# Optimization experiments

Measured on AMD Instinct MI355X. Metric: run time of the kernel, lower is better.

The kernel has to match this reference:

```python
import jax, jax.numpy as jnp
import numpy as np

DIM = 512
HIDDEN = 2048
BATCH = 16384
NUM_VECTORS = 3


def _mlp(z, W1, b1, W2, b2, W3, b3):
    # 3-layer tanh MLP: dim -> hidden -> hidden -> dim
    h = jnp.tanh(z @ W1.T + b1)
    h = jnp.tanh(h @ W2.T + b2)
    return h @ W3.T + b3


def setup_inputs() -> dict:
    key = jax.random.key(0)
    ks = jax.random.split(key, 10)
    t = jnp.zeros((1,), dtype=jnp.float32)
    augmented_state = jax.random.normal(ks[0], (BATCH, DIM + 1), dtype=jnp.float32)
    epsilons = jax.random.normal(ks[1], (NUM_VECTORS, BATCH, DIM), dtype=jnp.float32)
    # Xavier-normal-ish init with gain 0.1 (final layer randomized instead of the
    # original zero-init so outputs/grads are non-trivial for kernel testing).
    def xavier(k, fan_out, fan_in, gain=0.1):
        std = gain * np.sqrt(2.0 / (fan_in + fan_out))
        return (jax.random.normal(k, (fan_out, fan_in), dtype=jnp.float32) * std)
    W1 = xavier(ks[2], HIDDEN, DIM)
    b1 = jnp.zeros((HIDDEN,), dtype=jnp.float32)
    W2 = xavier(ks[3], HIDDEN, HIDDEN)
    b2 = jnp.zeros((HIDDEN,), dtype=jnp.float32)
    W3 = xavier(ks[4], DIM, HIDDEN)
    b3 = jnp.zeros((DIM,), dtype=jnp.float32)
    return {"t": t, "augmented_state": augmented_state, "epsilons": epsilons,
            "W1": W1, "b1": b1, "W2": W2, "b2": b2, "W3": W3, "b3": b3}


def reference(t, augmented_state, epsilons, W1, b1, W2, b2, W3, b3):
    dim = W1.shape[1]
    z = augmented_state[:, :dim]                      # [B, dim]
    dz_dt = _mlp(z, W1, b1, W2, b2, W3, b3)           # [B, dim]
    # torch code computes g = d(sum f(z))/dz = J^T @ 1 (same for every loop
    # iteration since only epsilon is resampled), then averages (g * eps).sum(1).
    g = jax.grad(lambda zz: _mlp(zz, W1, b1, W2, b2, W3, b3).sum())(z)  # [B, dim]
    num_vectors = epsilons.shape[0]
    trace = jnp.einsum('kbd,bd->b', epsilons, g)[:, None] / num_vectors  # [B, 1]
    return jnp.concatenate([dz_dt, trace], axis=1)    # [B, dim+1]
```

## Files before the change

kernel.cpp:

```cpp
#include <hip/hip_runtime.h>
#include <hip/hip_bf16.h>
#include <stdint.h>

#define DIM 512
#define HIDDEN 2048
#define BATCH 16384

using bf16 = __hip_bfloat16;
typedef float f32x4 __attribute__((ext_vector_type(4)));
typedef short bf16x8 __attribute__((ext_vector_type(8)));

__device__ __forceinline__ float bf2f(bf16 x) { return __bfloat162float(x); }
__device__ __forceinline__ bf16 f2bf(float x) { return __float2bfloat16(x); }

__device__ __forceinline__ float fast_tanh(float x) {
    float e = __expf(2.0f * x);
    return 1.0f - 2.0f * __builtin_amdgcn_rcpf(e + 1.0f);
}

__device__ __forceinline__ f32x4 mfma16(bf16x8 a, bf16x8 b, f32x4 c) {
    return __builtin_amdgcn_mfma_f32_16x16x32_bf16(a, b, c, 0, 0, 0);
}

__device__ __forceinline__ void BARP() {
    __builtin_amdgcn_sched_barrier(0);
    __builtin_amdgcn_s_barrier();
    __builtin_amdgcn_sched_barrier(0);
}
__device__ __forceinline__ void LGK0_SB() {
    asm volatile("s_waitcnt lgkmcnt(0)" ::: "memory");
    __builtin_amdgcn_sched_barrier(0);
}
__device__ __forceinline__ void VMC4() {
    asm volatile("s_waitcnt vmcnt(4)" ::: "memory");
}

__device__ __forceinline__ void stage_half(const bf16* __restrict__ G, int grow0,
                                           int Kdim, int kbase, bf16* lds,
                                           int elem_base, int wave, int srow4, int gs8)
{
#pragma unroll
    for (int i = 0; i < 2; ++i) {
        const int q = wave * 2 + i;
        const bf16* ga = G + (size_t)(grow0 + q * 16 + srow4) * Kdim + kbase + gs8;
        __builtin_amdgcn_global_load_lds(
            (const __attribute__((address_space(1))) void*)ga,
            (__attribute__((address_space(3))) void*)(lds + elem_base + q * 512), 16, 0, 0);
    }
}

template <int MODE>
__global__ __launch_bounds__(512, 2)
void gemm8(const bf16* __restrict__ A, const bf16* __restrict__ Bt,
           int M, int N, int K,
           const float* __restrict__ bias,
           bf16* __restrict__ out1, bf16* __restrict__ out2,
           const float* __restrict__ u3, const bf16* __restrict__ h1s)
{
    __shared__ bf16 lds[65536];
    const int tid  = threadIdx.x;
    const int lane = tid & 63;
    const int wave = tid >> 6;

    const int nwg = gridDim.x * gridDim.y;
    const int bid = blockIdx.y * gridDim.x + blockIdx.x;
    const int cpx = nwg >> 3;
    const int sw  = (bid & 7) * cpx + (bid >> 3);
    const int nbn = N >> 8;
    const int bm  = sw / nbn;
    const int bn  = sw % nbn;
    const int row0 = bm << 8;
    const int col0 = bn << 8;

    const int wr = wave >> 2;
    const int wc = wave & 3;
    const int l15 = lane & 15;

    const int slotl    = (((lane >> 4) ^ ((l15 >> 1) & 3)) << 4);
    const int laneoffA = (wr * 128 + l15) * 64 + slotl;
    const int laneoffB = (wc * 64  + l15) * 64 + slotl;
    const int srow4 = lane >> 2;
    const int gs8   = (((lane & 3) ^ ((lane >> 3) & 3)) << 3);

    const char* ldsc = (const char*)lds;
    f32x4 acc[8][4] = {};
    bf16x8 af[4], bfv[4];

    stage_half(A,  row0, K, 0,  lds, 0,     wave, srow4, gs8);
    stage_half(Bt, col0, K, 0,  lds, 16384, wave, srow4, gs8);
    stage_half(A,  row0, K, 32, lds, 8192,  wave, srow4, gs8);
    stage_half(Bt, col0, K, 32, lds, 24576, wave, srow4, gs8);
    VMC4(); BARP();

    const int KT = K >> 6;
    for (int t = 0; t < KT; ++t) {
        const int cur = t & 1;
        const int cb  = cur << 16;
        const int ce  = (cur ^ 1) << 15;
        const int knt = ((t + 1 < KT) ? t + 1 : 0) << 6;

#pragma unroll
        for (int j = 0; j < 4; ++j)
            af[j] = *(const bf16x8*)(ldsc + cb + j * 1024 + laneoffA);
#pragma unroll
        for (int j = 0; j < 4; ++j)
            bfv[j] = *(const bf16x8*)(ldsc + cb + 32768 + j * 1024 + laneoffB);
        stage_half(A, row0, K, knt, lds, ce, wave, srow4, gs8);
        BARP(); LGK0_SB();
        __builtin_amdgcn_s_setprio(1);
#pragma unroll
        for (int m = 0; m < 4; ++m)
#pragma unroll
            for (int n = 0; n < 4; ++n)
                acc[m][n] = mfma16(af[m], bfv[n], acc[m][n]);
        __builtin_amdgcn_s_setprio(0);
        BARP();

#pragma unroll
        for (int j = 0; j < 4; ++j)
            af[j] = *(const bf16x8*)(ldsc + cb + (4 + j) * 1024 + laneoffA);
        stage_half(Bt, col0, K, knt, lds, ce + 16384, wave, srow4, gs8);
        BARP(); LGK0_SB();
        __builtin_amdgcn_s_setprio(1);
#pragma unroll
        for (int m = 0; m < 4; ++m)
#pragma unroll
            for (int n = 0; n < 4; ++n)
                acc[4 + m][n] = mfma16(af[m], bfv[n], acc[4 + m][n]);
        __builtin_amdgcn_s_setprio(0);
        VMC4();
        BARP();

#pragma unroll
        for (int j = 0; j < 4; ++j)
            af[j] = *(const bf16x8*)(ldsc + cb + 16384 + j * 1024 + laneoffA);
#pragma unroll
        for (int j = 0; j < 4; ++j)
            bfv[j] = *(const bf16x8*)(ldsc + cb + 49152 + j * 1024 + laneoffB);
        stage_half(A, row0, K, knt + 32, lds, ce + 8192, wave, srow4, gs8);
        BARP(); LGK0_SB();
        __builtin_amdgcn_s_setprio(1);
#pragma unroll
        for (int m = 0; m < 4; ++m)
#pragma unroll
            for (int n = 0; n < 4; ++n)
                acc[m][n] = mfma16(af[m], bfv[n], acc[m][n]);
        __builtin_amdgcn_s_setprio(0);
        BARP();

#pragma unroll
        for (int j = 0; j < 4; ++j)
            af[j] = *(const bf16x8*)(ldsc + cb + 16384 + (4 + j) * 1024 + laneoffA);
        stage_half(Bt, col0, K, knt + 32, lds, ce + 24576, wave, srow4, gs8);
        BARP(); LGK0_SB();
        __builtin_amdgcn_s_setprio(1);
#pragma unroll
        for (int m = 0; m < 4; ++m)
#pragma unroll
            for (int n = 0; n < 4; ++n)
                acc[4 + m][n] = mfma16(af[m], bfv[n], acc[4 + m][n]);
        __builtin_amdgcn_s_setprio(0);
        VMC4();
        BARP();
    }

    const int c4 = (lane >> 4) << 2;
#pragma unroll
    for (int m = 0; m < 8; ++m) {
        const int growb = row0 + wr * 128 + m * 16 + c4;
#pragma unroll
        for (int n = 0; n < 4; ++n) {
            const int gcol = col0 + wc * 64 + n * 16 + l15;
            const float bz = (MODE == 3) ? 0.0f : bias[gcol];
            const float uu = (MODE == 1) ? u3[gcol] : 0.0f;
#pragma unroll
            for (int r = 0; r < 4; ++r) {
                const size_t idx = (size_t)(growb + r) * N + gcol;
                const float cv = acc[m][n][r];
                if (MODE == 0) {
                    out1[idx] = f2bf(fast_tanh(cv + bz));
                } else if (MODE == 1) {
                    float v = fast_tanh(cv + bz);
                    out1[idx] = f2bf(v);
                    out2[idx] = f2bf(uu * (1.0f - v * v));
                } else {
                    float h = bf2f(h1s[idx]);
                    out1[idx] = f2bf(cv * (1.0f - h * h));
                }
            }
        }
    }
}

template <int MODE>
__global__ __launch_bounds__(256)
void gemm_bt(const bf16* __restrict__ A, const bf16* __restrict__ Bt,
             int M, int N, int K,
             const float* __restrict__ bias,
             float* __restrict__ outF,
             const float* __restrict__ esum)
{
    __shared__ __align__(128) bf16 As[128 * 64];
    __shared__ __align__(128) bf16 Bs[128 * 64];

    const int tid  = threadIdx.x;
    const int lane = tid & 63;
    const int wave = tid >> 6;

    const int nwg = gridDim.x * gridDim.y;
    const int bid = blockIdx.y * gridDim.x + blockIdx.x;
    const int cpx = nwg >> 3;
    const int sw  = (bid & 7) * cpx + (bid >> 3);
    const int nbn = N >> 7;
    const int bm  = sw / nbn;
    const int bn  = sw % nbn;
    const int row0 = bm << 7;
    const int col0 = bn << 7;

    const int wr = wave >> 1;
    const int wc = wave & 1;

    f32x4 acc[4][4] = {};

    const int srow  = lane >> 3;
    const int sslot = lane & 7;

    const int KT = K >> 6;
    for (int kt = 0; kt < KT; ++kt) {
        const int k0 = kt << 6;
        __syncthreads();
#pragma unroll
        for (int i = 0; i < 4; ++i) {
            const int q   = wave * 4 + i;
            const int row = q * 8 + srow;
            const int gs  = sslot ^ (row & 7);
            const bf16* ga = A  + (size_t)(row0 + row) * K + (k0 + gs * 8);
            const bf16* gb = Bt + (size_t)(col0 + row) * K + (k0 + gs * 8);
            __builtin_amdgcn_global_load_lds(
                (const __attribute__((address_space(1))) void*)ga,
                (__attribute__((address_space(3))) void*)(As + q * 512), 16, 0, 0);
            __builtin_amdgcn_global_load_lds(
                (const __attribute__((address_space(1))) void*)gb,
                (__attribute__((address_space(3))) void*)(Bs + q * 512), 16, 0, 0);
        }
        __syncthreads();

#pragma unroll
        for (int half = 0; half < 2; ++half) {
            const int kb = half * 4 + (lane >> 4);
            bf16x8 af[4], bfr[4];
#pragma unroll
            for (int m = 0; m < 4; ++m) {
                const int ar = wr * 64 + m * 16 + (lane & 15);
                af[m] = *(const bf16x8*)((const char*)As + ar * 128 + ((kb ^ (ar & 7)) << 4));
            }
#pragma unroll
            for (int n = 0; n < 4; ++n) {
                const int br = wc * 64 + n * 16 + (lane & 15);
                bfr[n] = *(const bf16x8*)((const char*)Bs + br * 128 + ((kb ^ (br & 7)) << 4));
            }
#pragma unroll
            for (int m = 0; m < 4; ++m)
#pragma unroll
                for (int n = 0; n < 4; ++n)
                    acc[m][n] = mfma16(af[m], bfr[n], acc[m][n]);
        }
    }

    const int c_lo = lane & 15;
    const int c_hi = lane >> 4;
    if (MODE == 2) {
#pragma unroll
        for (int m = 0; m < 4; ++m)
#pragma unroll
            for (int n = 0; n < 4; ++n)
#pragma unroll
                for (int r = 0; r < 4; ++r) {
                    const int grow = row0 + wr * 64 + m * 16 + c_hi * 4 + r;
                    const int gcol = col0 + wc * 64 + n * 16 + c_lo;
                    outF[(size_t)grow * 513 + gcol] = acc[m][n][r] + bias[gcol];
                }
    } else {
#pragma unroll
        for (int m = 0; m < 4; ++m) {
#pragma unroll
            for (int r = 0; r < 4; ++r) {
                const int grow = row0 + wr * 64 + m * 16 + c_hi * 4 + r;
                float s = 0.f;
#pragma unroll
                for (int n = 0; n < 4; ++n) {
                    const int gcol = col0 + wc * 64 + n * 16 + c_lo;
                    s += acc[m][n][r] * esum[(size_t)grow * 512 + gcol];
                }
                s += __shfl_xor(s, 1);
                s += __shfl_xor(s, 2);
                s += __shfl_xor(s, 4);
                s += __shfl_xor(s, 8);
                if (c_lo == 0)
                    atomicAdd(outF + (size_t)grow * 513 + 512, s * (1.0f / 3.0f));
            }
        }
    }
}


__global__ void eps_reduce(const float* __restrict__ eps, float* __restrict__ esum, int n)
{
    const float4* e0 = (const float4*)eps;
    const float4* e1 = (const float4*)(eps + (size_t)n);
    const float4* e2 = (const float4*)(eps + 2 * (size_t)n);
    float4* o = (float4*)esum;
    const int n4 = n >> 2;
    const int stride = gridDim.x * blockDim.x;
    for (int i = blockIdx.x * blockDim.x + threadIdx.x; i < n4; i += stride) {
        float4 a = e0[i], b = e1[i], c = e2[i];
        o[i] = make_float4(a.x + b.x + c.x, a.y + b.y + c.y,
                           a.z + b.z + c.z, a.w + b.w + c.w);
    }
}

__global__ void z_convert(const float* __restrict__ aug, bf16* __restrict__ zb,
                          float* __restrict__ out)
{
    const int stride = gridDim.x * blockDim.x;
    for (int i = blockIdx.x * blockDim.x + threadIdx.x; i < BATCH * DIM; i += stride) {
        const int b = i >> 9, d = i & 511;
        zb[i] = f2bf(aug[(size_t)b * 513 + d]);
        if (d == 0) out[(size_t)b * 513 + 512] = 0.f;
    }
}

__global__ void conv_bf16(const float* __restrict__ src, bf16* __restrict__ dst, int n)
{
    const int stride = gridDim.x * blockDim.x;
    for (int i = blockIdx.x * blockDim.x + threadIdx.x; i < n; i += stride)
        dst[i] = f2bf(src[i]);
}

__global__ void transpose_bf16(const float* __restrict__ src, bf16* __restrict__ dst,
                               int R, int C)
{
    __shared__ float t[32][33];
    const int bx = blockIdx.x * 32;
    const int by = blockIdx.y * 32;
    const int tx = threadIdx.x & 31;
    const int ty = threadIdx.x >> 5;
#pragma unroll
    for (int j = 0; j < 32; j += 8)
        t[ty + j][tx] = src[(size_t)(by + ty + j) * C + (bx + tx)];
    __syncthreads();
#pragma unroll
    for (int j = 0; j < 32; j += 8)
        dst[(size_t)(bx + ty + j) * R + (by + tx)] = f2bf(t[tx][ty + j]);
}

__global__ void colsum(const float* __restrict__ W3, float* __restrict__ u3)
{
    const int j = blockIdx.x * blockDim.x + threadIdx.x;
    if (j >= HIDDEN) return;
    float s = 0.f;
    for (int i = 0; i < DIM; ++i) s += W3[(size_t)i * HIDDEN + j];
    u3[j] = s;
}

extern "C" void kernel_launch(void* const* d_in, const int* in_sizes, int n_in,
                              void* d_out, int out_size, void* d_ws, size_t ws_size,
                              hipStream_t stream)
{
    const float* aug = (const float*)d_in[1];
    const float* eps = (const float*)d_in[2];
    const float* W1  = (const float*)d_in[3];
    const float* b1  = (const float*)d_in[4];
    const float* W2  = (const float*)d_in[5];
    const float* b2  = (const float*)d_in[6];
    const float* W3  = (const float*)d_in[7];
    const float* b3  = (const float*)d_in[8];
    float* out = (float*)d_out;

    char* ws = (char*)d_ws;
    size_t off = 0;
    auto alloc = [&](size_t bytes) {
        char* p = ws + off;
        off += (bytes + 255) & ~(size_t)255;
        return p;
    };
    bf16*  zb   = (bf16*)alloc((size_t)BATCH * DIM * 2);
    bf16*  h1   = (bf16*)alloc((size_t)BATCH * HIDDEN * 2);
    bf16*  h2   = (bf16*)alloc((size_t)BATCH * HIDDEN * 2);
    bf16*  d2   = (bf16*)alloc((size_t)BATCH * HIDDEN * 2);
    float* esum = (float*)alloc((size_t)BATCH * DIM * 4);
    bf16*  W1b  = (bf16*)alloc((size_t)HIDDEN * DIM * 2);
    bf16*  W2b  = (bf16*)alloc((size_t)HIDDEN * HIDDEN * 2);
    bf16*  W3b  = (bf16*)alloc((size_t)DIM * HIDDEN * 2);
    bf16*  W2t  = (bf16*)alloc((size_t)HIDDEN * HIDDEN * 2);
    bf16*  W1t  = (bf16*)alloc((size_t)DIM * HIDDEN * 2);
    float* u3   = (float*)alloc((size_t)HIDDEN * 4);
    bf16*  d1   = h2;

    eps_reduce<<<2048, 256, 0, stream>>>(eps, esum, BATCH * DIM);
    z_convert<<<2048, 256, 0, stream>>>(aug, zb, out);
    conv_bf16<<<1024, 256, 0, stream>>>(W1, W1b, HIDDEN * DIM);
    conv_bf16<<<2048, 256, 0, stream>>>(W2, W2b, HIDDEN * HIDDEN);
    conv_bf16<<<1024, 256, 0, stream>>>(W3, W3b, DIM * HIDDEN);
    transpose_bf16<<<dim3(HIDDEN / 32, HIDDEN / 32), 256, 0, stream>>>(W2, W2t, HIDDEN, HIDDEN);
    transpose_bf16<<<dim3(DIM / 32, HIDDEN / 32), 256, 0, stream>>>(W1, W1t, HIDDEN, DIM);
    colsum<<<HIDDEN / 256, 256, 0, stream>>>(W3, u3);

    dim3 g8(BATCH / 256, HIDDEN / 256);
    dim3 gSml(BATCH / 128, DIM / 128);
    gemm8<0><<<g8, 512, 0, stream>>>(zb, W1b, BATCH, HIDDEN, DIM, b1,
                                     h1, nullptr, nullptr, nullptr);
    gemm8<1><<<g8, 512, 0, stream>>>(h1, W2b, BATCH, HIDDEN, HIDDEN, b2,
                                     h2, d2, u3, nullptr);
    gemm_bt<2><<<gSml, 256, 0, stream>>>(h2, W3b, BATCH, DIM, HIDDEN, b3, out, nullptr);
    gemm8<3><<<g8, 512, 0, stream>>>(d2, W2t, BATCH, HIDDEN, HIDDEN, nullptr,
                                     d1, nullptr, nullptr, h1);
    gemm_bt<4><<<gSml, 256, 0, stream>>>(d1, W1t, BATCH, DIM, HIDDEN, nullptr, out, esum);
}
```

Measured before the change: 666.2 us.

## Restructure GEMM main loop into register-prefetched pipeline with one barrier per k-tile

Replaces the four-phase loop, which had a barrier before each MFMA group, with a pipeline that prefetches the next LDS fragments into a second set of registers while the current MFMAs run. Partial lgkmcnt waits replace full drains, and all global-to-LDS staging for tile t+2 is issued after a single barrier per k-tile. The aim is to cut barrier stalls and hide LDS read latency behind MFMA work. The cost is more live registers (four fragment arrays), which may pressure occupancy, and a full vmcnt(0) drain each iteration.

After: 667.5 us. No clear change (+0.2%).

```diff
diff --git a/kernel.cpp b/kernel.cpp
--- a/kernel.cpp
+++ b/kernel.cpp
@@ -27,13 +27,9 @@
     __builtin_amdgcn_s_barrier();
     __builtin_amdgcn_sched_barrier(0);
 }
-__device__ __forceinline__ void LGK0_SB() {
-    asm volatile("s_waitcnt lgkmcnt(0)" ::: "memory");
-    __builtin_amdgcn_sched_barrier(0);
-}
-__device__ __forceinline__ void VMC4() {
-    asm volatile("s_waitcnt vmcnt(4)" ::: "memory");
-}
+#define LGKM(N) do { asm volatile("s_waitcnt lgkmcnt(" #N ")" ::: "memory"); \
+                     __builtin_amdgcn_sched_barrier(0); } while (0)
+#define VMCNT(N) asm volatile("s_waitcnt vmcnt(" #N ")" ::: "memory")
 
 __device__ __forceinline__ void stage_half(const bf16* __restrict__ G, int grow0,
                                            int Kdim, int kbase, bf16* lds,
@@ -84,84 +80,95 @@
 
     const char* ldsc = (const char*)lds;
     f32x4 acc[8][4] = {};
-    bf16x8 af[4], bfv[4];
+    bf16x8 A03[4], A47[4], B0[4], B1[4];
+
+    const int KT = K >> 6;
 
     stage_half(A,  row0, K, 0,  lds, 0,     wave, srow4, gs8);
     stage_half(Bt, col0, K, 0,  lds, 16384, wave, srow4, gs8);
     stage_half(A,  row0, K, 32, lds, 8192,  wave, srow4, gs8);
     stage_half(Bt, col0, K, 32, lds, 24576, wave, srow4, gs8);
-    VMC4(); BARP();
-
-    const int KT = K >> 6;
+    stage_half(A,  row0, K, 64, lds, 32768 + 0,     wave, srow4, gs8);
+    stage_half(Bt, col0, K, 64, lds, 32768 + 16384, wave, srow4, gs8);
+    stage_half(A,  row0, K, 96, lds, 32768 + 8192,  wave, srow4, gs8);
+    stage_half(Bt, col0, K, 96, lds, 32768 + 24576, wave, srow4, gs8);
+    VMCNT(8);
+    BARP();
+#pragma unroll
+    for (int j = 0; j < 4; ++j)
+        A03[j] = *(const bf16x8*)(ldsc + j * 1024 + laneoffA);
+#pragma unroll
+    for (int j = 0; j < 4; ++j)
+        B0[j]  = *(const bf16x8*)(ldsc + 32768 + j * 1024 + laneoffB);
+
     for (int t = 0; t < KT; ++t) {
-        const int cur = t & 1;
-        const int cb  = cur << 16;
-        const int ce  = (cur ^ 1) << 15;
-        const int knt = ((t + 1 < KT) ? t + 1 : 0) << 6;
-
-#pragma unroll
-        for (int j = 0; j < 4; ++j)
-            af[j] = *(const bf16x8*)(ldsc + cb + j * 1024 + laneoffA);
-#pragma unroll
-        for (int j = 0; j < 4; ++j)
-            bfv[j] = *(const bf16x8*)(ldsc + cb + 32768 + j * 1024 + laneoffB);
-        stage_half(A, row0, K, knt, lds, ce, wave, srow4, gs8);
-        BARP(); LGK0_SB();
+        const int cb = (t & 1) << 16;
+
+#pragma unroll
+        for (int j = 0; j < 4; ++j)
+            A47[j] = *(const bf16x8*)(ldsc + cb + (4 + j) * 1024 + laneoffA);
+        LGKM(4);
         __builtin_amdgcn_s_setprio(1);
 #pragma unroll
         for (int m = 0; m < 4; ++m)
 #pragma unroll
             for (int n = 0; n < 4; ++n)
-                acc[m][n] = mfma16(af[m], bfv[n], acc[m][n]);
+                acc[m][n] = mfma16(A03[m], B0[n], acc[m][n]);
         __builtin_amdgcn_s_setprio(0);
+
+#pragma unroll
+        for (int j = 0; j < 4; ++j)
+            A03[j] = *(const bf16x8*)(ldsc + cb + 16384 + j * 1024 + laneoffA);
+#pragma unroll
+        for (int j = 0; j < 4; ++j)
+            B1[j]  = *(const bf16x8*)(ldsc + cb + 49152 + j * 1024 + laneoffB);
+        LGKM(8);
+        __builtin_amdgcn_s_setprio(1);
+#pragma unroll
+        for (int m = 0; m < 4; ++m)
+#pragma unroll
+            for (int n = 0; n < 4; ++n)
+                acc[4 + m][n] = mfma16(A47[m], B0[n], acc[4 + m][n]);
+        __builtin_amdgcn_s_setprio(0);
+
+#pragma unroll
+        for (int j = 0; j < 4; ++j)
+            A47[j] = *(const bf16x8*)(ldsc + cb + 16384 + (4 + j) * 1024 + laneoffA);
+        LGKM(4);
+        __builtin_amdgcn_s_setprio(1);
+#pragma unroll
+        for (int m = 0; m < 4; ++m)
+#pragma unroll
+            for (int n = 0; n < 4; ++n)
+                acc[m][n] = mfma16(A03[m], B1[n], acc[m][n]);
+        __builtin_amdgcn_s_setprio(0);
+
+        LGKM(0);
+        VMCNT(0);
         BARP();
 
-#pragma unroll
-        for (int j = 0; j < 4; ++j)
-            af[j] = *(const bf16x8*)(ldsc + cb + (4 + j) * 1024 + laneoffA);
-        stage_half(Bt, col0, K, knt, lds, ce + 16384, wave, srow4, gs8);
-        BARP(); LGK0_SB();
+        if (t + 2 < KT) {
+            const int k2  = (t + 2) << 6;
+            const int ceb = (t & 1) << 15;
+            stage_half(A,  row0, K, k2,      lds, ceb + 0,     wave, srow4, gs8);
+            stage_half(Bt, col0, K, k2,      lds, ceb + 16384, wave, srow4, gs8);
+            stage_half(A,  row0, K, k2 + 32, lds, ceb + 8192,  wave, srow4, gs8);
+            stage_half(Bt, col0, K, k2 + 32, lds, ceb + 24576, wave, srow4, gs8);
+        }
+        const int nb = ((t + 1) & 1) << 16;
+#pragma unroll
+        for (int j = 0; j < 4; ++j)
+            A03[j] = *(const bf16x8*)(ldsc + nb + j * 1024 + laneoffA);
+#pragma unroll
+        for (int j = 0; j < 4; ++j)
+            B0[j]  = *(const bf16x8*)(ldsc + nb + 32768 + j * 1024 + laneoffB);
         __builtin_amdgcn_s_setprio(1);
 #pragma unroll
         for (int m = 0; m < 4; ++m)
 #pragma unroll
             for (int n = 0; n < 4; ++n)
-                acc[4 + m][n] = mfma16(af[m], bfv[n], acc[4 + m][n]);
+                acc[4 + m][n] = mfma16(A47[m], B1[n], acc[4 + m][n]);
         __builtin_amdgcn_s_setprio(0);
-        VMC4();
-        BARP();
-
-#pragma unroll
-        for (int j = 0; j < 4; ++j)
-            af[j] = *(const bf16x8*)(ldsc + cb + 16384 + j * 1024 + laneoffA);
-#pragma unroll
-        for (int j = 0; j < 4; ++j)
-            bfv[j] = *(const bf16x8*)(ldsc + cb + 49152 + j * 1024 + laneoffB);
-        stage_half(A, row0, K, knt + 32, lds, ce + 8192, wave, srow4, gs8);
-        BARP(); LGK0_SB();
-        __builtin_amdgcn_s_setprio(1);
-#pragma unroll
-        for (int m = 0; m < 4; ++m)
-#pragma unroll
-            for (int n = 0; n < 4; ++n)
-                acc[m][n] = mfma16(af[m], bfv[n], acc[m][n]);
-        __builtin_amdgcn_s_setprio(0);
-        BARP();
-
-#pragma unroll
-        for (int j = 0; j < 4; ++j)
-            af[j] = *(const bf16x8*)(ldsc + cb + 16384 + (4 + j) * 1024 + laneoffA);
-        stage_half(Bt, col0, K, knt + 32, lds, ce + 24576, wave, srow4, gs8);
-        BARP(); LGK0_SB();
-        __builtin_amdgcn_s_setprio(1);
-#pragma unroll
-        for (int m = 0; m < 4; ++m)
-#pragma unroll
-            for (int n = 0; n < 4; ++n)
-                acc[4 + m][n] = mfma16(af[m], bfv[n], acc[4 + m][n]);
-        __builtin_amdgcn_s_setprio(0);
-        VMC4();
-        BARP();
     }
 
     const int c4 = (lane >> 4) << 2;
```
